# Performance work log

Hardware: AMD Instinct MI355X
Metric: run time of the kernel (lower is better)

Reference implementation:

```python
import jax, jax.numpy as jnp
import numpy as np

N_NODES = 50000
N_EDGES = 320000
B = 4096          # subgraph batch: users/items/subg nodes
IN_N = 64         # in_nfeats
IN_E = 16         # in_efeats
OUT_E = 2 * IN_E  # out_edge_feats = in_efeats*2
H = 4             # num_heads
D = 64            # latent dim per layer (latent_dim=[64,64])
L = 2             # num EGAT layers


def setup_inputs() -> dict:
    key = jax.random.key(0)
    ks = iter(jax.random.split(key, 48))
    def nrm(shape, s=0.05):
        return jax.random.normal(next(ks), shape, dtype=jnp.float32) * s
    inp = {}
    inp['x'] = jax.random.normal(next(ks), (N_NODES, IN_N), dtype=jnp.float32)
    inp['efeat'] = jax.random.normal(next(ks), (N_EDGES, IN_E), dtype=jnp.float32)
    inp['efeat2'] = jax.random.normal(next(ks), (N_EDGES, IN_N), dtype=jnp.float32)
    inp['edge_mask'] = (jax.random.uniform(next(ks), (N_EDGES,)) > 0.1).astype(jnp.float32)
    inp['edge_mask2'] = (jax.random.uniform(next(ks), (N_EDGES,)) > 0.1).astype(jnp.float32)
    inp['src'] = jax.random.randint(next(ks), (N_EDGES,), 0, N_NODES, dtype=jnp.int32)
    inp['dst'] = jax.random.randint(next(ks), (N_EDGES,), 0, N_NODES, dtype=jnp.int32)
    inp['user_idx'] = jnp.arange(0, B, dtype=jnp.int32)          # ntype==0
    inp['item_idx'] = jnp.arange(B, 2 * B, dtype=jnp.int32)      # ntype==1
    inp['subg_idx'] = jnp.arange(2 * B, 3 * B, dtype=jnp.int32)  # ntype==-1
    # stacked per-layer EGAT params (layer dims identical since IN_N == D)
    inp['loc_wni'] = nrm((L, D, H * OUT_E))
    inp['loc_wnj'] = nrm((L, D, H * OUT_E))
    inp['loc_we'] = nrm((L, IN_E, H * OUT_E))
    inp['loc_attn'] = nrm((L, H, OUT_E))
    inp['loc_wnode'] = nrm((L, D, H * D))
    inp['agg1_w'] = nrm((L, H * D, D))
    inp['agg1_b'] = jnp.zeros((L, D), jnp.float32)
    inp['glob_wni'] = nrm((L, D, H * OUT_E))
    inp['glob_wnj'] = nrm((L, D, H * OUT_E))
    inp['glob_we'] = nrm((L, IN_N, H * OUT_E))
    inp['glob_attn'] = nrm((L, H, OUT_E))
    inp['glob_wnode'] = nrm((L, D, H * D))
    inp['agg2_w'] = nrm((L, H * D, D))
    inp['agg2_b'] = jnp.zeros((L, D), jnp.float32)
    inp['w1_ui'] = nrm((2 * L * D, 128))
    inp['b1_ui'] = jnp.zeros((128,), jnp.float32)
    inp['w1_sg'] = nrm((L * D, 128))
    inp['b1_sg'] = jnp.zeros((128,), jnp.float32)
    inp['w2_ui'] = nrm((128, 1))
    inp['b2_ui'] = jnp.zeros((1,), jnp.float32)
    inp['w2_sg'] = nrm((128, 1))
    inp['b2_sg'] = jnp.zeros((1,), jnp.float32)
    return inp


def _egat(x, e, norm, src, dst, wni, wnj, we, attn, wnode):
    # edge feature: f_ij = LeakyReLU(W_ni x_i + W_nj x_j + W_e e_ij), slope 0.2 (DGL EGATConv)
    f = (x @ wni)[src] + (x @ wnj)[dst] + e @ we            # (E, H*OUT_E)
    f = jax.nn.leaky_relu(f.reshape(-1, H, OUT_E), 0.2)
    scores = jnp.einsum('ehd,hd->eh', f, attn)              # (E, H)
    # edge softmax over incoming edges of each dst node
    m = jax.ops.segment_max(scores, dst, num_segments=N_NODES)
    m = jnp.where(jnp.isfinite(m), m, 0.0)
    ex = jnp.exp(scores - m[dst])
    denom = jax.ops.segment_sum(ex, dst, num_segments=N_NODES)
    a = ex / (denom[dst] + 1e-9)
    a = a * norm[:, None]                                    # per-edge norm (edge mask) weighting
    fn = (x @ wnode).reshape(-1, H, D)                       # (N, H, D)
    msg = fn[src] * a[:, :, None]                            # (E, H, D)
    out = jax.ops.segment_sum(msg, dst, num_segments=N_NODES)
    return out, a


def reference(x, efeat, efeat2, edge_mask, edge_mask2, src, dst, user_idx, item_idx, subg_idx,
              loc_wni, loc_wnj, loc_we, loc_attn, loc_wnode, agg1_w, agg1_b,
              glob_wni, glob_wnj, glob_we, glob_attn, glob_wnode, agg2_w, agg2_b,
              w1_ui, b1_ui, w1_sg, b1_sg, w2_ui, b2_ui, w2_sg, b2_sg):
    h = x
    ui_states, sg_states = [], []
    for l in range(L):
        out, _ = _egat(h, efeat, edge_mask, src, dst,
                       loc_wni[l], loc_wnj[l], loc_we[l], loc_attn[l], loc_wnode[l])
        h = jax.nn.elu(out.reshape(N_NODES, H * D) @ agg1_w[l] + agg1_b[l])
        ui_states.append(h)
        out, _ = _egat(h, efeat2, edge_mask2, src, dst,
                       glob_wni[l], glob_wnj[l], glob_we[l], glob_attn[l], glob_wnode[l])
        h = jax.nn.leaky_relu(out.reshape(N_NODES, H * D) @ agg2_w[l] + agg2_b[l], 0.01)
        sg_states.append(h)
    ui = jnp.concatenate(ui_states, axis=1)   # (N, L*D)
    sg = jnp.concatenate(sg_states, axis=1)   # (N, L*D)
    ui_x = jnp.concatenate([ui[user_idx], ui[item_idx]], axis=1)  # (B, 2*L*D)
    sg_x = sg[subg_idx]                                           # (B, L*D)
    ui_h = jax.nn.relu(ui_x @ w1_ui + b1_ui)  # dropout is identity in eval
    sg_h = jax.nn.relu(sg_x @ w1_sg + b1_sg)
    ui_out = jax.nn.sigmoid(ui_h @ w2_ui + b2_ui)[:, 0]
    sg_out = jax.nn.sigmoid(sg_h @ w2_sg + b2_sg)[:, 0]
    return (sg_out, ui_out)
```

## Files before the change

kernel.cpp:

```cpp
#include <hip/hip_runtime.h>
#include <math.h>

#define NN 50000
#define NE 320000
#define BATCH 4096

typedef __bf16 bf16x8 __attribute__((ext_vector_type(8)));
typedef float floatx4 __attribute__((ext_vector_type(4)));
typedef float floatx16 __attribute__((ext_vector_type(16)));
typedef unsigned short ushort;
typedef unsigned int uint;

__device__ __forceinline__ float lrelu02(float x) { return x > 0.f ? x : 0.2f * x; }
__device__ __forceinline__ float b2f(ushort h) { return __uint_as_float(((uint)h) << 16); }
__device__ __forceinline__ float b2f_lo(uint u) { return __uint_as_float(u << 16); }
__device__ __forceinline__ float b2f_hi(uint u) { return __uint_as_float(u & 0xffff0000u); }
__device__ __forceinline__ ushort f2b(float x) {
    uint u = __float_as_uint(x);
    return (ushort)((u + 0x7fffu + ((u >> 16) & 1u)) >> 16);
}
__device__ __forceinline__ uint pk2(float a, float b) {
    return (uint)f2b(a) | ((uint)f2b(b) << 16);
}

template <int GLOB>
__global__ __launch_bounds__(512, 4) void score32(
    const float* __restrict__ ef,
    const ushort* __restrict__ Bfrag,
    const ushort* __restrict__ hb,
    const int* __restrict__ srcv, const int* __restrict__ dstv,
    const float* __restrict__ attn, float* __restrict__ scv)
{
    constexpr int NK = GLOB ? 12 : 9;
    constexpr int KTOT = NK * 16;
    constexpr int EFR = GLOB ? 4 : 1;
    constexpr int LDA = GLOB ? 64 : 16;
    __shared__ __align__(16) ushort As[128 * KTOT];
    const int tid = threadIdx.x;
    const int wid = tid >> 6, lane = tid & 63;
    const int hi = lane >> 5;
    const int row = (blockIdx.x << 8) + (wid << 5) + (lane & 31);

    const int s_n = srcv[row];
    const int d_n = dstv[row];

    bf16x8 bfr[NK];
#pragma unroll
    for (int t = 0; t < EFR; t++) {
        const float* ap = ef + (size_t)row * LDA + t * 16 + hi * 8;
        float4 f0 = *(const float4*)ap;
        float4 f1 = *(const float4*)(ap + 4);
        uint4 av;
        av.x = pk2(f0.x, f0.y); av.y = pk2(f0.z, f0.w);
        av.z = pk2(f1.x, f1.y); av.w = pk2(f1.z, f1.w);
        *(uint4*)&bfr[t] = av;
    }
#pragma unroll
    for (int t = 0; t < 4; t++)
        bfr[EFR + t] = *(const bf16x8*)(hb + (size_t)s_n * 64 + t * 16 + hi * 8);
#pragma unroll
    for (int t = 0; t < 4; t++)
        bfr[EFR + 4 + t] = *(const bf16x8*)(hb + (size_t)d_n * 64 + t * 16 + hi * 8);

    for (int i = tid; i < 128 * KTOT / 8; i += 512)
        *(uint4*)(As + (size_t)i * 8) = *(const uint4*)(Bfrag + (size_t)i * 8);
    __syncthreads();

    float ph[4];
#pragma unroll
    for (int c = 0; c < 4; c++) {
        floatx16 acc;
#pragma unroll
        for (int r = 0; r < 16; r++) acc[r] = 0.f;
#pragma unroll
        for (int t = 0; t < NK; t++) {
            bf16x8 afr = *(const bf16x8*)(As + ((size_t)(c * NK + t) * 64 + lane) * 8);
            acc = __builtin_amdgcn_mfma_f32_32x32x16_bf16(afr, bfr[t], acc, 0, 0, 0);
        }
        float v = 0.f;
#pragma unroll
        for (int q = 0; q < 4; q++) {
            float4 at4 = *(const float4*)(attn + c * 32 + hi * 4 + q * 8);
            v = fmaf(lrelu02(acc[q * 4 + 0]), at4.x, v);
            v = fmaf(lrelu02(acc[q * 4 + 1]), at4.y, v);
            v = fmaf(lrelu02(acc[q * 4 + 2]), at4.z, v);
            v = fmaf(lrelu02(acc[q * 4 + 3]), at4.w, v);
        }
        ph[c] = v;
    }
#pragma unroll
    for (int h = 0; h < 4; h++) ph[h] += __shfl_xor(ph[h], 32);
    if (hi == 0)
        *(float4*)(scv + (size_t)row * 4) = make_float4(ph[0], ph[1], ph[2], ph[3]);
}

__global__ __launch_bounds__(256) void gemm_agg(
    const ushort* __restrict__ A, int M,
    const ushort* __restrict__ Bt,
    const float* __restrict__ bias, int act,
    ushort* __restrict__ outb)
{
    __shared__ __align__(16) ushort Bs[64 * 264];
    const int tid = threadIdx.x;
    const int row0 = blockIdx.x << 6;
    const int w = tid >> 6, lane = tid & 63;
    const int quad = lane >> 4, l16 = lane & 15;
    const int arow = row0 + 16 * w + l16;

    for (int idx = tid; idx < 64 * 32; idx += 256) {
        int r = idx >> 5, c8 = (idx & 31) << 3;
        *(uint4*)(Bs + r * 264 + c8) = *(const uint4*)(Bt + (size_t)r * 256 + c8);
    }

    bf16x8 afr[8];
#pragma unroll
    for (int kt = 0; kt < 8; kt++) {
        uint4 av = make_uint4(0u, 0u, 0u, 0u);
        if (arow < M)
            av = *(const uint4*)(A + (size_t)arow * 256 + kt * 32 + quad * 8);
        *(uint4*)&afr[kt] = av;
    }
    __syncthreads();

    floatx4 acc[4];
#pragma unroll
    for (int c = 0; c < 4; c++)
#pragma unroll
        for (int r = 0; r < 4; r++) acc[c][r] = 0.f;

#pragma unroll
    for (int kt = 0; kt < 8; kt++) {
#pragma unroll
        for (int c = 0; c < 4; c++) {
            bf16x8 bfv = *(const bf16x8*)(Bs + (16 * c + l16) * 264 + kt * 32 + quad * 8);
            acc[c] = __builtin_amdgcn_mfma_f32_16x16x32_bf16(afr[kt], bfv, acc[c], 0, 0, 0);
        }
    }
#pragma unroll
    for (int r = 0; r < 4; r++) {
        int gr = row0 + 16 * w + quad * 4 + r;
        if (gr < M) {
#pragma unroll
            for (int c = 0; c < 4; c++) {
                int col = 16 * c + l16;
                float v = acc[c][r] + bias[col];
                if (act == 0) v = v > 0.f ? v : (__expf(v) - 1.f);
                else          v = v > 0.f ? v : 0.01f * v;
                outb[(size_t)gr * 64 + col] = f2b(v);
            }
        }
    }
}

__global__ void k_count(const int* __restrict__ dst, int* __restrict__ deg, int E)
{
    for (int i = blockIdx.x * blockDim.x + threadIdx.x; i < E; i += gridDim.x * blockDim.x)
        atomicAdd(&deg[dst[i]], 1);
}

__global__ __launch_bounds__(256) void scan_local(
    const int* __restrict__ deg, int* __restrict__ rowptr, int* __restrict__ partials, int N)
{
    __shared__ int sd[256];
    int tid = threadIdx.x;
    int i = blockIdx.x * 256 + tid;
    int v = (i < N) ? deg[i] : 0;
    sd[tid] = v; __syncthreads();
#pragma unroll
    for (int off = 1; off < 256; off <<= 1) {
        int t = (tid >= off) ? sd[tid - off] : 0;
        __syncthreads();
        sd[tid] += t;
        __syncthreads();
    }
    if (i < N) rowptr[i] = sd[tid] - v;
    if (tid == 255) partials[blockIdx.x] = sd[255];
}

__global__ __launch_bounds__(256) void scan_partials(int* __restrict__ partials, int nb)
{
    __shared__ int sd[256];
    int tid = threadIdx.x;
    int v = (tid < nb) ? partials[tid] : 0;
    sd[tid] = v; __syncthreads();
#pragma unroll
    for (int off = 1; off < 256; off <<= 1) {
        int t = (tid >= off) ? sd[tid - off] : 0;
        __syncthreads();
        sd[tid] += t;
        __syncthreads();
    }
    if (tid < nb) partials[tid] = sd[tid] - v;
}

__global__ void scan_add(int* __restrict__ rowptr, const int* __restrict__ partials, int N, int E)
{
    int i = blockIdx.x * 256 + threadIdx.x;
    if (i < N) rowptr[i] += partials[i >> 8];
    if (i == 0) rowptr[N] = E;
}

__global__ void k_scatter(const int* __restrict__ dst, const int* __restrict__ rowptr,
                          int* __restrict__ cnt, int* __restrict__ eidx, int E)
{
    for (int i = blockIdx.x * blockDim.x + threadIdx.x; i < E; i += gridDim.x * blockDim.x) {
        int d = dst[i];
        int p = rowptr[d] + atomicAdd(&cnt[d], 1);
        eidx[p] = i;
    }
}

__global__ void k_sort_buckets(const int* __restrict__ rowptr, int* __restrict__ eidx, int N)
{
    int n = blockIdx.x * blockDim.x + threadIdx.x;
    if (n >= N) return;
    int beg = rowptr[n], end = rowptr[n + 1];
    for (int i = beg + 1; i < end; i++) {
        int v = eidx[i];
        int j = i - 1;
        while (j >= beg && eidx[j] > v) { eidx[j + 1] = eidx[j]; j--; }
        eidx[j + 1] = v;
    }
}

__global__ void k_perm_small(const int* __restrict__ eidx, const int* __restrict__ src,
                             const float* __restrict__ m1, const float* __restrict__ m2,
                             int* __restrict__ srcp, float* __restrict__ m1p,
                             float* __restrict__ m2p, int E)
{
    int p = blockIdx.x * blockDim.x + threadIdx.x;
    if (p < E) {
        int e = eidx[p];
        srcp[p] = src[e];
        m1p[p] = m1[e];
        m2p[p] = m2[e];
    }
}

__global__ void k_cvt(const float* __restrict__ in, ushort* __restrict__ out, int n)
{
    for (int i = blockIdx.x * blockDim.x + threadIdx.x; i < n; i += gridDim.x * blockDim.x)
        out[i] = f2b(in[i]);
}

__global__ void k_prep_score_all(const float* __restrict__ loc_we, const float* __restrict__ glob_we,
                                 const float* __restrict__ loc_wni, const float* __restrict__ glob_wni,
                                 const float* __restrict__ loc_wnj, const float* __restrict__ glob_wnj,
                                 ushort* __restrict__ B)
{
    int idx = blockIdx.x * 256 + threadIdx.x;
    if (idx >= 4 * 24576) return;
    int e = idx / 24576, rem = idx % 24576;
    int layer = e >> 1, gl = e & 1;
    int NK = gl ? 12 : 9;
    int KTOT = NK * 16;
    int ef_end = gl ? 64 : 16;
    if (rem >= 128 * KTOT) return;
    int j = rem & 7, lane = (rem >> 3) & 63, tf = rem >> 9;
    int c = tf / NK, t = tf % NK;
    int m = 32 * c + (lane & 31);
    int k = 16 * t + 8 * (lane >> 5) + j;
    const float* we  = (gl ? glob_we  + layer * 64 * 128 : loc_we  + layer * 16 * 128);
    const float* wni = (gl ? glob_wni : loc_wni) + layer * 64 * 128;
    const float* wnj = (gl ? glob_wnj : loc_wnj) + layer * 64 * 128;
    float v;
    if (k < ef_end)            v = we[k * 128 + m];
    else if (k < ef_end + 64)  v = wni[(k - ef_end) * 128 + m];
    else                       v = wnj[(k - ef_end - 64) * 128 + m];
    B[e * 24576 + rem] = f2b(v);
}

__global__ void k_fold_all(const float* __restrict__ loc_wnode, const float* __restrict__ agg1_w,
                           const float* __restrict__ glob_wnode, const float* __restrict__ agg2_w,
                           ushort* __restrict__ B)
{
    int e = blockIdx.x >> 6;
    int idx = (blockIdx.x & 63) * 256 + threadIdx.x;
    int layer = e >> 1, gl = e & 1;
    const float* wnode = (gl ? glob_wnode : loc_wnode) + layer * 64 * 256;
    const float* aggw  = (gl ? agg2_w : agg1_w) + layer * 256 * 64;
    int j = idx >> 8, col = idx & 255;
    int h = col >> 6, ii = col & 63;
    float s = 0.f;
#pragma unroll 8
    for (int k = 0; k < 64; k++)
        s = fmaf(wnode[ii * 256 + h * 64 + k], aggw[(h * 64 + k) * 64 + j], s);
    B[e * 16384 + j * 256 + col] = f2b(s);
}

__global__ __launch_bounds__(256) void node_fused(
    const float* __restrict__ scv,
    const int* __restrict__ eidx,
    const int* __restrict__ rowptr, const int* __restrict__ srcp,
    const float* __restrict__ maskp,
    const ushort* __restrict__ hsrc,
    ushort* __restrict__ zb)
{
    int tid = threadIdx.x;
    int n = (blockIdx.x << 5) | (tid >> 3);
    int sl = tid & 7;
    if (n >= NN) return;
    int beg = rowptr[n], end = rowptr[n + 1];
    float l0 = 0.f, l1 = 0.f, l2 = 0.f, l3 = 0.f;
    float acc[4][8] = {};
#pragma unroll 4
    for (int i = beg; i < end; i++) {
        int ep = eidx[i];
        float4 s4 = *(const float4*)(scv + (size_t)ep * 4);
        float mk = maskp[i];
        int s = srcp[i];
        uint4 hvv = *(const uint4*)(hsrc + (size_t)s * 64 + sl * 8);
        float t0 = __expf(s4.x), t1 = __expf(s4.y), t2 = __expf(s4.z), t3 = __expf(s4.w);
        l0 += t0; l1 += t1; l2 += t2; l3 += t3;
        float a0 = t0 * mk, a1 = t1 * mk, a2 = t2 * mk, a3 = t3 * mk;
        float hv[8] = { b2f_lo(hvv.x), b2f_hi(hvv.x), b2f_lo(hvv.y), b2f_hi(hvv.y),
                        b2f_lo(hvv.z), b2f_hi(hvv.z), b2f_lo(hvv.w), b2f_hi(hvv.w) };
#pragma unroll
        for (int c = 0; c < 8; c++) {
            acc[0][c] = fmaf(a0, hv[c], acc[0][c]);
            acc[1][c] = fmaf(a1, hv[c], acc[1][c]);
            acc[2][c] = fmaf(a2, hv[c], acc[2][c]);
            acc[3][c] = fmaf(a3, hv[c], acc[3][c]);
        }
    }
    float inv[4] = { 1.f / (l0 + 1e-9f), 1.f / (l1 + 1e-9f),
                     1.f / (l2 + 1e-9f), 1.f / (l3 + 1e-9f) };
#pragma unroll
    for (int h = 0; h < 4; h++) {
        uint4 o;
        o.x = pk2(acc[h][0] * inv[h], acc[h][1] * inv[h]);
        o.y = pk2(acc[h][2] * inv[h], acc[h][3] * inv[h]);
        o.z = pk2(acc[h][4] * inv[h], acc[h][5] * inv[h]);
        o.w = pk2(acc[h][6] * inv[h], acc[h][7] * inv[h]);
        *(uint4*)(zb + (size_t)n * 256 + h * 64 + sl * 8) = o;
    }
}

__global__ __launch_bounds__(256) void final_ui(
    const ushort* __restrict__ s0, const ushort* __restrict__ s1,
    const int* __restrict__ uidx, const int* __restrict__ iidx,
    const float* __restrict__ w1, const float* __restrict__ b1,
    const float* __restrict__ w2, const float* __restrict__ b2, float* __restrict__ out)
{
    __shared__ float xs[4][256];
    int tid = threadIdx.x, wid = tid >> 6, lane = tid & 63;
    int r = (blockIdx.x << 2) + wid;
    int u = uidx[r], it = iidx[r];
    xs[wid][lane]       = b2f(s0[(size_t)u * 64 + lane]);
    xs[wid][64 + lane]  = b2f(s1[(size_t)u * 64 + lane]);
    xs[wid][128 + lane] = b2f(s0[(size_t)it * 64 + lane]);
    xs[wid][192 + lane] = b2f(s1[(size_t)it * 64 + lane]);
    __syncthreads();
    int c = lane << 1;
    float a0 = b1[c], a1 = b1[c + 1];
    for (int k = 0; k < 256; k++) {
        float xv = xs[wid][k];
        float2 wv = *(const float2*)(w1 + (size_t)k * 128 + c);
        a0 = fmaf(xv, wv.x, a0);
        a1 = fmaf(xv, wv.y, a1);
    }
    a0 = fmaxf(a0, 0.f);
    a1 = fmaxf(a1, 0.f);
    float2 w2v = *(const float2*)(w2 + c);
    float p = a0 * w2v.x + a1 * w2v.y;
#pragma unroll
    for (int mm = 1; mm < 64; mm <<= 1) p += __shfl_xor(p, mm);
    if (lane == 0) out[r] = 1.f / (1.f + __expf(-(p + b2[0])));
}

__global__ __launch_bounds__(256) void final_sg(
    const ushort* __restrict__ s0, const ushort* __restrict__ s1,
    const int* __restrict__ gidx,
    const float* __restrict__ w1, const float* __restrict__ b1,
    const float* __restrict__ w2, const float* __restrict__ b2, float* __restrict__ out)
{
    __shared__ float xs[4][128];
    int tid = threadIdx.x, wid = tid >> 6, lane = tid & 63;
    int r = (blockIdx.x << 2) + wid;
    int n = gidx[r];
    xs[wid][lane]      = b2f(s0[(size_t)n * 64 + lane]);
    xs[wid][64 + lane] = b2f(s1[(size_t)n * 64 + lane]);
    __syncthreads();
    int c = lane << 1;
    float a0 = b1[c], a1 = b1[c + 1];
    for (int k = 0; k < 128; k++) {
        float xv = xs[wid][k];
        float2 wv = *(const float2*)(w1 + (size_t)k * 128 + c);
        a0 = fmaf(xv, wv.x, a0);
        a1 = fmaf(xv, wv.y, a1);
    }
    a0 = fmaxf(a0, 0.f);
    a1 = fmaxf(a1, 0.f);
    float2 w2v = *(const float2*)(w2 + c);
    float p = a0 * w2v.x + a1 * w2v.y;
#pragma unroll
    for (int mm = 1; mm < 64; mm <<= 1) p += __shfl_xor(p, mm);
    if (lane == 0) out[r] = 1.f / (1.f + __expf(-(p + b2[0])));
}

extern "C" void kernel_launch(void* const* d_in, const int* in_sizes, int n_in,
                              void* d_out, int out_size, void* d_ws, size_t ws_size,
                              hipStream_t stream)
{
    const float* x       = (const float*)d_in[0];
    const float* efeat   = (const float*)d_in[1];
    const float* efeat2  = (const float*)d_in[2];
    const float* mask1   = (const float*)d_in[3];
    const float* mask2   = (const float*)d_in[4];
    const int*   src     = (const int*)d_in[5];
    const int*   dst     = (const int*)d_in[6];
    const int*   uidx    = (const int*)d_in[7];
    const int*   iidx    = (const int*)d_in[8];
    const int*   gidx    = (const int*)d_in[9];
    const float* loc_wni = (const float*)d_in[10];
    const float* loc_wnj = (const float*)d_in[11];
    const float* loc_we  = (const float*)d_in[12];
    const float* loc_attn= (const float*)d_in[13];
    const float* loc_wnode=(const float*)d_in[14];
    const float* agg1_w  = (const float*)d_in[15];
    const float* agg1_b  = (const float*)d_in[16];
    const float* glob_wni= (const float*)d_in[17];
    const float* glob_wnj= (const float*)d_in[18];
    const float* glob_we = (const float*)d_in[19];
    const float* glob_attn=(const float*)d_in[20];
    const float* glob_wnode=(const float*)d_in[21];
    const float* agg2_w  = (const float*)d_in[22];
    const float* agg2_b  = (const float*)d_in[23];
    const float* w1_ui   = (const float*)d_in[24];
    const float* b1_ui   = (const float*)d_in[25];
    const float* w1_sg   = (const float*)d_in[26];
    const float* b1_sg   = (const float*)d_in[27];
    const float* w2_ui   = (const float*)d_in[28];
    const float* b2_ui   = (const float*)d_in[29];
    const float* w2_sg   = (const float*)d_in[30];
    const float* b2_sg   = (const float*)d_in[31];

    char* wsp = (char*)d_ws;
    auto carve = [&](size_t bytes) { char* p = wsp; wsp += (bytes + 255) & ~(size_t)255; return p; };
    ushort* zb    = (ushort*)carve((size_t)NN * 256 * 2);
    ushort* hb[5];
    for (int i = 0; i < 5; i++) hb[i] = (ushort*)carve((size_t)NN * 64 * 2);
    float*  scv   = (float*)carve((size_t)NE * 16);
    float*  m1p   = (float*)carve((size_t)NE * 4);
    float*  m2p   = (float*)carve((size_t)NE * 4);
    int*    srcp  = (int*)carve((size_t)NE * 4);
    int*    eidx  = (int*)carve((size_t)NE * 4);
    ushort* Bsc   = (ushort*)carve(4 * 24576 * 2);
    ushort* Bfold = (ushort*)carve(4 * 16384 * 2);
    int* deg      = (int*)carve(NN * 4);
    int* rowptr   = (int*)carve((NN + 4) * 4);
    int* partials = (int*)carve(256 * 4);

    k_prep_score_all<<<384, 256, 0, stream>>>(loc_we, glob_we, loc_wni, glob_wni,
                                              loc_wnj, glob_wnj, Bsc);
    k_fold_all<<<256, 256, 0, stream>>>(loc_wnode, agg1_w, glob_wnode, agg2_w, Bfold);
    hipMemsetAsync(deg, 0, NN * sizeof(int), stream);
    k_count<<<1280, 256, 0, stream>>>(dst, deg, NE);
    scan_local<<<196, 256, 0, stream>>>(deg, rowptr, partials, NN);
    scan_partials<<<1, 256, 0, stream>>>(partials, 196);
    scan_add<<<196, 256, 0, stream>>>(rowptr, partials, NN, NE);
    hipMemsetAsync(deg, 0, NN * sizeof(int), stream);
    k_scatter<<<1280, 256, 0, stream>>>(dst, rowptr, deg, eidx, NE);
    k_sort_buckets<<<196, 256, 0, stream>>>(rowptr, eidx, NN);
    k_perm_small<<<1250, 256, 0, stream>>>(eidx, src, mask1, mask2,
                                           srcp, m1p, m2p, NE);
    k_cvt<<<3200, 256, 0, stream>>>(x, hb[0], NN * 64);

    auto egat = [&](const ushort* hin, int e, const float* maskp, const float* attn,
                    const float* aggb, int act, ushort* hout) {
        int is_glob = e & 1;
        if (is_glob)
            score32<1><<<1250, 512, 0, stream>>>(efeat2, Bsc + e * 24576, hin,
                                                 src, dst, attn, scv);
        else
            score32<0><<<1250, 512, 0, stream>>>(efeat, Bsc + e * 24576, hin,
                                                 src, dst, attn, scv);
        node_fused<<<(NN + 31) / 32, 256, 0, stream>>>(scv, eidx, rowptr, srcp, maskp, hin, zb);
        gemm_agg<<<782, 256, 0, stream>>>(zb, NN, Bfold + e * 16384, aggb, act, hout);
    };

    egat(hb[0], 0, m1p, loc_attn,        agg1_b,      0, hb[1]);
    egat(hb[1], 1, m2p, glob_attn,       agg2_b,      1, hb[2]);
    egat(hb[2], 2, m1p, loc_attn + 128,  agg1_b + 64, 0, hb[3]);
    egat(hb[3], 3, m2p, glob_attn + 128, agg2_b + 64, 1, hb[4]);

    float* out = (float*)d_out;
    final_sg<<<BATCH / 4, 256, 0, stream>>>(hb[2], hb[4], gidx, w1_sg, b1_sg, w2_sg, b2_sg, out);
    final_ui<<<BATCH / 4, 256, 0, stream>>>(hb[1], hb[3], uidx, iidx, w1_ui, b1_ui, w2_ui, b2_ui, out + BATCH);
}
```

Measured before the change: 568.1 us.

## Fuse node aggregation with folded aggregation GEMM via shared-memory staging

Merges the per-node softmax-weighted neighbor aggregation kernel and the following MFMA GEMM into one kernel. Each 512-thread block aggregates 64 nodes into a bf16 tile in LDS, then eight waves compute the 64x64 output with MFMA. This removes the global write and re-read of the 50000x256 bf16 intermediate and one launch per layer. The cost is higher LDS use per block (about 67 KB) and a block-wide barrier, so waves on nodes with few edges wait for those with many before the GEMM starts.

```diff
diff --git a/kernel.cpp b/kernel.cpp
--- a/kernel.cpp
+++ b/kernel.cpp
@@ -94,56 +94,95 @@
         *(float4*)(scv + (size_t)row * 4) = make_float4(ph[0], ph[1], ph[2], ph[3]);
 }
 
-__global__ __launch_bounds__(256) void gemm_agg(
-    const ushort* __restrict__ A, int M,
+__global__ __launch_bounds__(512, 2) void node_gemm(
+    const float* __restrict__ scv,
+    const int* __restrict__ eidx,
+    const int* __restrict__ rowptr, const int* __restrict__ srcp,
+    const float* __restrict__ maskp,
+    const ushort* __restrict__ hsrc,
     const ushort* __restrict__ Bt,
     const float* __restrict__ bias, int act,
     ushort* __restrict__ outb)
 {
+    __shared__ __align__(16) ushort Zs[64 * 264];
     __shared__ __align__(16) ushort Bs[64 * 264];
     const int tid = threadIdx.x;
-    const int row0 = blockIdx.x << 6;
+    const int n0 = blockIdx.x << 6;
+
+    for (int idx = tid; idx < 64 * 32; idx += 512) {
+        int r = idx >> 5, c8 = (idx & 31) << 3;
+        *(uint4*)(Bs + r * 264 + c8) = *(const uint4*)(Bt + (size_t)r * 256 + c8);
+    }
+
+    {
+        int ln = tid >> 3, sl = tid & 7;
+        int n = n0 + ln;
+        float l0 = 0.f, l1 = 0.f, l2 = 0.f, l3 = 0.f;
+        float acc[4][8] = {};
+        if (n < NN) {
+            int beg = rowptr[n], end = rowptr[n + 1];
+#pragma unroll 4
+            for (int i = beg; i < end; i++) {
+                int ep = eidx[i];
+                float4 s4 = *(const float4*)(scv + (size_t)ep * 4);
+                float mk = maskp[i];
+                int s = srcp[i];
+                uint4 hvv = *(const uint4*)(hsrc + (size_t)s * 64 + sl * 8);
+                float t0 = __expf(s4.x), t1 = __expf(s4.y), t2 = __expf(s4.z), t3 = __expf(s4.w);
+                l0 += t0; l1 += t1; l2 += t2; l3 += t3;
+                float a0 = t0 * mk, a1 = t1 * mk, a2 = t2 * mk, a3 = t3 * mk;
+                float hv[8] = { b2f_lo(hvv.x), b2f_hi(hvv.x), b2f_lo(hvv.y), b2f_hi(hvv.y),
+                                b2f_lo(hvv.z), b2f_hi(hvv.z), b2f_lo(hvv.w), b2f_hi(hvv.w) };
+#pragma unroll
+                for (int c = 0; c < 8; c++) {
+                    acc[0][c] = fmaf(a0, hv[c], acc[0][c]);
+                    acc[1][c] = fmaf(a1, hv[c], acc[1][c]);
+                    acc[2][c] = fmaf(a2, hv[c], acc[2][c]);
+                    acc[3][c] = fmaf(a3, hv[c], acc[3][c]);
+                }
+            }
+        }
+        float inv[4] = { 1.f / (l0 + 1e-9f), 1.f / (l1 + 1e-9f),
+                         1.f / (l2 + 1e-9f), 1.f / (l3 + 1e-9f) };
+#pragma unroll
+        for (int h = 0; h < 4; h++) {
+            uint4 o;
+            o.x = pk2(acc[h][0] * inv[h], acc[h][1] * inv[h]);
+            o.y = pk2(acc[h][2] * inv[h], acc[h][3] * inv[h]);
+            o.z = pk2(acc[h][4] * inv[h], acc[h][5] * inv[h]);
+            o.w = pk2(acc[h][6] * inv[h], acc[h][7] * inv[h]);
+            *(uint4*)(Zs + ln * 264 + h * 64 + sl * 8) = o;
+        }
+    }
+    __syncthreads();
+
     const int w = tid >> 6, lane = tid & 63;
     const int quad = lane >> 4, l16 = lane & 15;
-    const int arow = row0 + 16 * w + l16;
-
-    for (int idx = tid; idx < 64 * 32; idx += 256) {
-        int r = idx >> 5, c8 = (idx & 31) << 3;
-        *(uint4*)(Bs + r * 264 + c8) = *(const uint4*)(Bt + (size_t)r * 256 + c8);
-    }
-
-    bf16x8 afr[8];
+    const int rw = w & 3, cp = w >> 2;
+
+    floatx4 acc2[2];
+#pragma unroll
+    for (int cc = 0; cc < 2; cc++)
+#pragma unroll
+        for (int r = 0; r < 4; r++) acc2[cc][r] = 0.f;
+
 #pragma unroll
     for (int kt = 0; kt < 8; kt++) {
-        uint4 av = make_uint4(0u, 0u, 0u, 0u);
-        if (arow < M)
-            av = *(const uint4*)(A + (size_t)arow * 256 + kt * 32 + quad * 8);
-        *(uint4*)&afr[kt] = av;
-    }
-    __syncthreads();
-
-    floatx4 acc[4];
-#pragma unroll
-    for (int c = 0; c < 4; c++)
-#pragma unroll
-        for (int r = 0; r < 4; r++) acc[c][r] = 0.f;
-
-#pragma unroll
-    for (int kt = 0; kt < 8; kt++) {
-#pragma unroll
-        for (int c = 0; c < 4; c++) {
-            bf16x8 bfv = *(const bf16x8*)(Bs + (16 * c + l16) * 264 + kt * 32 + quad * 8);
-            acc[c] = __builtin_amdgcn_mfma_f32_16x16x32_bf16(afr[kt], bfv, acc[c], 0, 0, 0);
+        bf16x8 af = *(const bf16x8*)(Zs + (16 * rw + l16) * 264 + kt * 32 + quad * 8);
+#pragma unroll
+        for (int cc = 0; cc < 2; cc++) {
+            bf16x8 bfv = *(const bf16x8*)(Bs + (16 * (2 * cp + cc) + l16) * 264 + kt * 32 + quad * 8);
+            acc2[cc] = __builtin_amdgcn_mfma_f32_16x16x32_bf16(af, bfv, acc2[cc], 0, 0, 0);
         }
     }
 #pragma unroll
     for (int r = 0; r < 4; r++) {
-        int gr = row0 + 16 * w + quad * 4 + r;
-        if (gr < M) {
-#pragma unroll
-            for (int c = 0; c < 4; c++) {
-                int col = 16 * c + l16;
-                float v = acc[c][r] + bias[col];
+        int gr = n0 + 16 * rw + quad * 4 + r;
+        if (gr < NN) {
+#pragma unroll
+            for (int cc = 0; cc < 2; cc++) {
+                int col = 16 * (2 * cp + cc) + l16;
+                float v = acc2[cc][r] + bias[col];
                 if (act == 0) v = v > 0.f ? v : (__expf(v) - 1.f);
                 else          v = v > 0.f ? v : 0.01f * v;
                 outb[(size_t)gr * 64 + col] = f2b(v);
@@ -286,54 +325,6 @@
     for (int k = 0; k < 64; k++)
         s = fmaf(wnode[ii * 256 + h * 64 + k], aggw[(h * 64 + k) * 64 + j], s);
     B[e * 16384 + j * 256 + col] = f2b(s);
-}
-
-__global__ __launch_bounds__(256) void node_fused(
-    const float* __restrict__ scv,
-    const int* __restrict__ eidx,
-    const int* __restrict__ rowptr, const int* __restrict__ srcp,
-    const float* __restrict__ maskp,
-    const ushort* __restrict__ hsrc,
-    ushort* __restrict__ zb)
-{
-    int tid = threadIdx.x;
-    int n = (blockIdx.x << 5) | (tid >> 3);
-    int sl = tid & 7;
-    if (n >= NN) return;
-    int beg = rowptr[n], end = rowptr[n + 1];
-    float l0 = 0.f, l1 = 0.f, l2 = 0.f, l3 = 0.f;
-    float acc[4][8] = {};
-#pragma unroll 4
-    for (int i = beg; i < end; i++) {
-        int ep = eidx[i];
-        float4 s4 = *(const float4*)(scv + (size_t)ep * 4);
-        float mk = maskp[i];
-        int s = srcp[i];
-        uint4 hvv = *(const uint4*)(hsrc + (size_t)s * 64 + sl * 8);
-        float t0 = __expf(s4.x), t1 = __expf(s4.y), t2 = __expf(s4.z), t3 = __expf(s4.w);
-        l0 += t0; l1 += t1; l2 += t2; l3 += t3;
-        float a0 = t0 * mk, a1 = t1 * mk, a2 = t2 * mk, a3 = t3 * mk;
-        float hv[8] = { b2f_lo(hvv.x), b2f_hi(hvv.x), b2f_lo(hvv.y), b2f_hi(hvv.y),
-                        b2f_lo(hvv.z), b2f_hi(hvv.z), b2f_lo(hvv.w), b2f_hi(hvv.w) };
-#pragma unroll
-        for (int c = 0; c < 8; c++) {
-            acc[0][c] = fmaf(a0, hv[c], acc[0][c]);
-            acc[1][c] = fmaf(a1, hv[c], acc[1][c]);
-            acc[2][c] = fmaf(a2, hv[c], acc[2][c]);
-            acc[3][c] = fmaf(a3, hv[c], acc[3][c]);
-        }
-    }
-    float inv[4] = { 1.f / (l0 + 1e-9f), 1.f / (l1 + 1e-9f),
-                     1.f / (l2 + 1e-9f), 1.f / (l3 + 1e-9f) };
-#pragma unroll
-    for (int h = 0; h < 4; h++) {
-        uint4 o;
-        o.x = pk2(acc[h][0] * inv[h], acc[h][1] * inv[h]);
-        o.y = pk2(acc[h][2] * inv[h], acc[h][3] * inv[h]);
-        o.z = pk2(acc[h][4] * inv[h], acc[h][5] * inv[h]);
-        o.w = pk2(acc[h][6] * inv[h], acc[h][7] * inv[h]);
-        *(uint4*)(zb + (size_t)n * 256 + h * 64 + sl * 8) = o;
-    }
 }
 
 __global__ __launch_bounds__(256) void final_ui(
@@ -437,7 +428,6 @@
 
     char* wsp = (char*)d_ws;
     auto carve = [&](size_t bytes) { char* p = wsp; wsp += (bytes + 255) & ~(size_t)255; return p; };
-    ushort* zb    = (ushort*)carve((size_t)NN * 256 * 2);
     ushort* hb[5];
     for (int i = 0; i < 5; i++) hb[i] = (ushort*)carve((size_t)NN * 64 * 2);
     float*  scv   = (float*)carve((size_t)NE * 16);
@@ -475,8 +465,9 @@
         else
             score32<0><<<1250, 512, 0, stream>>>(efeat, Bsc + e * 24576, hin,
                                                  src, dst, attn, scv);
-        node_fused<<<(NN + 31) / 32, 256, 0, stream>>>(scv, eidx, rowptr, srcp, maskp, hin, zb);
-        gemm_agg<<<782, 256, 0, stream>>>(zb, NN, Bfold + e * 16384, aggb, act, hout);
+        node_gemm<<<(NN + 63) / 64, 512, 0, stream>>>(scv, eidx, rowptr, srcp, maskp,
+                                                      hin, Bfold + e * 16384, aggb,
+                                                      act, hout);
     };
 
     egat(hb[0], 0, m1p, loc_attn,        agg1_b,      0, hb[1]);
```

Result: faster. 545.8 us (-3.9%).
